# Kernel tuning notes

Hardware: AMD Instinct MI355X
Metric: run time of the kernel (lower is better)

## Reference

```python
import jax, jax.numpy as jnp
import numpy as np

D = 128; DFF = 256; NH = 4; HD = D // NH
B = 8; T = 1024
PAIRS = [(0, 1), (1, 2), (0, 2)]  # (ABSTRACT,DYNAMIC),(DYNAMIC,CONCRETE),(ABSTRACT,CONCRETE)
BW = 0.5 / 3.0   # bridge_weight / len(BRIDGE_PAIRS)
LB_W = 0.01


def _hex_np():
    # itertools.product([-1,1], repeat=6): index i = 6-bit binary of i, MSB first, 0->-1
    bits = (np.arange(64)[:, None] >> np.arange(5, -1, -1)) & 1
    return (bits * 2.0 - 1.0).astype(np.float32)


def _anchors_np():
    h = _hex_np()
    idx = {'GEO': 0, 'HYDRO': 18, 'PYRO': 45, 'AERO': 6, 'COSMO': 27, 'NOOS': 63}
    a = (h[idx['NOOS']] + h[idx['COSMO']]) / 2.0   # ABSTRACT
    d = (h[idx['AERO']] + h[idx['PYRO']]) / 2.0    # DYNAMIC
    c = (h[idx['GEO']] + h[idx['HYDRO']]) / 2.0    # CONCRETE
    return np.stack([a, d, c]).astype(np.float32)


def _ln(x, g, b, eps=1e-5):
    m = x.mean(-1, keepdims=True)
    v = ((x - m) ** 2).mean(-1, keepdims=True)
    return (x - m) * jax.lax.rsqrt(v + eps) * g + b


def _mha(q, kv, in_w, out_w):
    # torch nn.MultiheadAttention, bias=False, batch_first
    Bq, Tq, _ = q.shape
    wq, wk, wv = in_w[:D], in_w[D:2 * D], in_w[2 * D:]
    Q = (q @ wq.T).reshape(Bq, Tq, NH, HD)
    K = (kv @ wk.T).reshape(Bq, Tq, NH, HD)
    V = (kv @ wv.T).reshape(Bq, Tq, NH, HD)
    scores = jnp.einsum('bqhd,bkhd->bhqk', Q, K) / jnp.sqrt(jnp.float32(HD))
    attn = jax.nn.softmax(scores, axis=-1)
    o = jnp.einsum('bhqk,bkhd->bqhd', attn, V).reshape(Bq, Tq, D)
    return o @ out_w.T


def setup_inputs() -> dict:
    key = jax.random.key(0)
    ks = iter(jax.random.split(key, 40))
    r = lambda shape, s=0.02: jax.random.normal(next(ks), shape, dtype=jnp.float32) * s
    return {
        'x': jax.random.normal(next(ks), (B, T, D), dtype=jnp.float32),
        'gr_norm_g': jnp.ones((D,), jnp.float32), 'gr_norm_b': jnp.zeros((D,), jnp.float32),
        'q6_w': r((6, D), 0.1),
        'log_temp': jnp.log(jnp.float32(0.5)),
        'grp_norm_g': jnp.ones((3, D), jnp.float32), 'grp_norm_b': jnp.zeros((3, D), jnp.float32),
        'grp_proj_w': r((3, 2, D), 0.1), 'grp_proj_b': jnp.zeros((3, 2), jnp.float32),
        'me_norm_g': jnp.ones((6, D), jnp.float32), 'me_norm_b': jnp.zeros((6, D), jnp.float32),
        'me_gate_w': r((6, DFF, D)), 'me_val_w': r((6, DFF, D)), 'me_out_w': r((6, D, DFF)),
        'br_in_w': r((3, 3 * D, D)), 'br_out_w': r((3, D, D)),
        'br_nq_g': jnp.ones((3, D), jnp.float32), 'br_nq_b': jnp.zeros((3, D), jnp.float32),
        'br_nkv_g': jnp.ones((3, D), jnp.float32), 'br_nkv_b': jnp.zeros((3, D), jnp.float32),
        'br_nffn_g': jnp.ones((3, D), jnp.float32), 'br_nffn_b': jnp.zeros((3, D), jnp.float32),
        'br_gate_w': r((3, 2 * D, D)), 'br_val_w': r((3, 2 * D, D)), 'br_ffn_out_w': r((3, D, 2 * D)),
        'br_gate': jnp.full((3,), -2.0, dtype=jnp.float32),
        'out_norm_g': jnp.ones((D,), jnp.float32), 'out_norm_b': jnp.zeros((D,), jnp.float32),
        'out_w': r((D, D)),
    }


def reference(x, gr_norm_g, gr_norm_b, q6_w, log_temp, grp_norm_g, grp_norm_b,
              grp_proj_w, grp_proj_b, me_norm_g, me_norm_b, me_gate_w, me_val_w,
              me_out_w, br_in_w, br_out_w, br_nq_g, br_nq_b, br_nkv_g, br_nkv_b,
              br_nffn_g, br_nffn_b, br_gate_w, br_val_w, br_ffn_out_w, br_gate,
              out_norm_g, out_norm_b, out_w):
    hexg = jnp.asarray(_hex_np())        # (64, 6)
    anchors = jnp.asarray(_anchors_np())  # (3, 6)

    # ---- GlobalRouter ----
    h = _ln(x, gr_norm_g, gr_norm_b)
    soft_bits = jnp.tanh(h @ q6_w.T)                       # (B,T,6)
    sim = soft_bits @ hexg.T                               # (B,T,64)
    temp = jnp.clip(jnp.exp(log_temp), 0.1, 5.0)
    hex_w = jax.nn.softmax(sim / temp, axis=-1)
    soft_hex = hex_w @ hexg                                # (B,T,6)
    group_weights = jax.nn.softmax(soft_hex @ anchors.T, axis=-1)  # (B,T,3)
    mw = group_weights.mean(axis=(0, 1))
    lb_total = -(mw * jnp.log(mw + 1e-8)).sum()

    # ---- all 6 micro experts (per-expert LayerNorm shares x's stats) ----
    m = x.mean(-1, keepdims=True)
    v = ((x - m) ** 2).mean(-1, keepdims=True)
    xn = (x - m) * jax.lax.rsqrt(v + 1e-5)                 # (B,T,D)
    hme = xn[None] * me_norm_g[:, None, None, :] + me_norm_b[:, None, None, :]  # (6,B,T,D)
    gate = jax.nn.silu(jnp.einsum('ebtd,efd->ebtf', hme, me_gate_w))
    val = jnp.einsum('ebtd,efd->ebtf', hme, me_val_w)
    eo = jnp.einsum('ebtf,edf->ebtd', gate * val, me_out_w)  # (6,B,T,D)

    # ---- per-group routing (2 experts each, top_k=2) ----
    group_outs = []
    for g in range(3):  # groups ordered [ABSTRACT, DYNAMIC, CONCRETE]; experts [2g, 2g+1]
        hg = xn * grp_norm_g[g] + grp_norm_b[g]
        logits = hg @ grp_proj_w[g].T + grp_proj_b[g]      # (B,T,2)
        w = jax.nn.softmax(logits, axis=-1)
        vals, idx = jax.lax.top_k(w, 2)                    # k = min(top_k=2, n=2)
        sparse = (jax.nn.one_hot(idx, 2, dtype=w.dtype) * vals[..., None]).sum(-2)
        sparse = sparse / (sparse.sum(-1, keepdims=True) + 1e-8)
        mwg = w.mean(axis=(0, 1))
        lb_total = lb_total - (mwg * jnp.log(mwg + 1e-8)).sum()
        go = sparse[..., 0:1] * eo[2 * g] + sparse[..., 1:2] * eo[2 * g + 1]
        group_outs.append(group_weights[..., g:g + 1] * go)

    # ---- bridge experts ----
    bridge_sum = jnp.zeros_like(x)
    for i, (a, b) in enumerate(PAIRS):
        xq, xk = group_outs[a], group_outs[b]
        qn = _ln(xq, br_nq_g[i], br_nq_b[i])
        kvn = _ln(xk, br_nkv_g[i], br_nkv_b[i])
        xb = xq + _mha(qn, kvn, br_in_w[i], br_out_w[i])
        hb = _ln(xb, br_nffn_g[i], br_nffn_b[i])
        ff = (jax.nn.silu(hb @ br_gate_w[i].T) * (hb @ br_val_w[i].T)) @ br_ffn_out_w[i].T
        xb = (xb + ff) * jax.nn.sigmoid(br_gate[i])
        bridge_sum = bridge_sum + BW * xb

    combined = group_outs[0] + group_outs[1] + group_outs[2] + bridge_sum
    out = _ln(combined, out_norm_g, out_norm_b) @ out_w.T
    return out, lb_total * LB_W
```

## Files before the change

kernel.cpp:

```cpp
#include <hip/hip_runtime.h>
#include <math.h>

#define DD    128
#define DFF   256
#define NHH   4
#define HDD   32
#define BB    8
#define TT    1024
#define NTOK  (BB*TT)
#define LDK   72
#define QKVN  384

#define WB_MEGATE 0
#define WB_MEVAL  196608
#define WB_MEOUT  393216
#define WB_BRIN   589824
#define WB_BROUT  737280
#define WB_BRG    786432
#define WB_BRV    884736
#define WB_BRF    983040
#define WB_OUTW   1081344
#define WB_TOT    1097728

typedef __bf16 bf16x8 __attribute__((ext_vector_type(8)));
typedef float  f32x4  __attribute__((ext_vector_type(4)));

__device__ __forceinline__ float wsum(float v){
#pragma unroll
  for(int o=32;o>0;o>>=1) v += __shfl_xor(v,o,64);
  return v;
}
__device__ __forceinline__ float wmaxr(float v){
#pragma unroll
  for(int o=32;o>0;o>>=1) v = fmaxf(v,__shfl_xor(v,o,64));
  return v;
}
__device__ __forceinline__ unsigned short f2bf(float x){
  __bf16 h = (__bf16)x;
  unsigned short u;
  __builtin_memcpy(&u, &h, 2);
  return u;
}

__device__ __forceinline__ void stage16(const float* __restrict__ gp,
                                        unsigned short* __restrict__ dst){
  float4 f0 = *reinterpret_cast<const float4*>(gp);
  float4 f1 = *reinterpret_cast<const float4*>(gp+4);
  float4 f2 = *reinterpret_cast<const float4*>(gp+8);
  float4 f3 = *reinterpret_cast<const float4*>(gp+12);
  float f[16] = {f0.x,f0.y,f0.z,f0.w, f1.x,f1.y,f1.z,f1.w,
                 f2.x,f2.y,f2.z,f2.w, f3.x,f3.y,f3.z,f3.w};
  unsigned short h[16];
#pragma unroll
  for(int j=0;j<16;j++) h[j] = f2bf(f[j]);
  *reinterpret_cast<uint4*>(dst)   = *reinterpret_cast<const uint4*>(h);
  *reinterpret_cast<uint4*>(dst+8) = *reinterpret_cast<const uint4*>(h+8);
}

__device__ __forceinline__ void stage16bf(const unsigned short* __restrict__ gp,
                                          unsigned short* __restrict__ dst){
  const uint4* s = reinterpret_cast<const uint4*>(gp);
  *reinterpret_cast<uint4*>(dst)   = s[0];
  *reinterpret_cast<uint4*>(dst+8) = s[1];
}

__device__ __forceinline__ void stageLN(const float* __restrict__ fr,
                                        float mean, float rstd,
                                        const float* __restrict__ g,
                                        const float* __restrict__ b,
                                        unsigned short* __restrict__ dst){
  unsigned short h[16];
#pragma unroll
  for(int j=0;j<16;j++){
    float y = (fr[j]-mean)*rstd*g[j] + b[j];
    h[j] = f2bf(y);
  }
  *reinterpret_cast<uint4*>(dst)   = *reinterpret_cast<const uint4*>(h);
  *reinterpret_cast<uint4*>(dst+8) = *reinterpret_cast<const uint4*>(h+8);
}

__global__ __launch_bounds__(256) void wconv(
    const float* __restrict__ a0, const float* __restrict__ a1, const float* __restrict__ a2,
    const float* __restrict__ a3, const float* __restrict__ a4, const float* __restrict__ a5,
    const float* __restrict__ a6, const float* __restrict__ a7, const float* __restrict__ a8,
    unsigned short* __restrict__ dst, float qsc){
  size_t i = ((size_t)blockIdx.x*256 + threadIdx.x)*4;
  if(i >= WB_TOT) return;
  const float* s; size_t off = i; float sc = 1.0f;
  if(i < WB_MEVAL){ s=a0; }
  else if(i < WB_MEOUT){ s=a1; off = i-WB_MEVAL; }
  else if(i < WB_BRIN ){ s=a2; off = i-WB_MEOUT; }
  else if(i < WB_BROUT){ s=a3; off = i-WB_BRIN;
    int row = (int)(off>>7); if((row % 384) < 128) sc = qsc; }
  else if(i < WB_BRG ){ s=a4; off = i-WB_BROUT; }
  else if(i < WB_BRV ){ s=a5; off = i-WB_BRG; }
  else if(i < WB_BRF ){ s=a6; off = i-WB_BRV; }
  else if(i < WB_OUTW){ s=a7; off = i-WB_BRF; }
  else { s=a8; off = i-WB_OUTW; }
  float4 v = *reinterpret_cast<const float4*>(s + off);
  unsigned short h4[4] = {f2bf(v.x*sc), f2bf(v.y*sc), f2bf(v.z*sc), f2bf(v.w*sc)};
  *reinterpret_cast<uint2*>(dst + i) = *reinterpret_cast<const uint2*>(h4);
}

__global__ __launch_bounds__(256) void routing_kernel(
    const float* __restrict__ x,
    const float* __restrict__ gr_g, const float* __restrict__ gr_b,
    const float* __restrict__ q6,   const float* __restrict__ logtemp,
    const float* __restrict__ grp_g,const float* __restrict__ grp_b,
    const float* __restrict__ gpw,  const float* __restrict__ gpb,
    float* __restrict__ gw_out, float* __restrict__ coef, float* __restrict__ part){
  __shared__ float sp[4][9];
  int lane = threadIdx.x & 63;
  int wv   = threadIdx.x >> 6;
  int t    = (blockIdx.x<<2) + wv;
  const float* xr = x + (size_t)t*DD;
  float r0 = xr[lane], r1 = xr[lane+64];
  float mn = wsum(r0+r1) * (1.0f/DD);
  float d0 = r0-mn, d1 = r1-mn;
  float vv = wsum(d0*d0 + d1*d1) * (1.0f/DD);
  float rstd = rsqrtf(vv + 1e-5f);
  float x0 = d0*rstd, x1 = d1*rstd;
  float h0 = x0*gr_g[lane]+gr_b[lane];
  float h1 = x1*gr_g[lane+64]+gr_b[lane+64];
  float sb[6];
#pragma unroll
  for(int j=0;j<6;j++){
    float p = h0*q6[j*DD+lane] + h1*q6[j*DD+lane+64];
    sb[j] = tanhf(wsum(p));
  }
  float sim = 0.f;
#pragma unroll
  for(int j=0;j<6;j++) sim += ((lane>>(5-j))&1) ? sb[j] : -sb[j];
  float temp = expf(logtemp[0]); temp = fminf(fmaxf(temp,0.1f),5.0f);
  float mx = wmaxr(sim);
  float p  = expf((sim-mx)/temp);
  float w  = p / wsum(p);
  float sh[6];
#pragma unroll
  for(int j=0;j<6;j++) sh[j] = wsum(((lane>>(5-j))&1) ? w : -w);
  const float A0[6]={0,1,1,0,1,1}, A1[6]={0,-1,0,1,0,0}, A2[6]={-1,0,-1,-1,0,-1};
  float l0=0,l1=0,l2=0;
#pragma unroll
  for(int j=0;j<6;j++){ l0+=sh[j]*A0[j]; l1+=sh[j]*A1[j]; l2+=sh[j]*A2[j]; }
  float m3 = fmaxf(l0,fmaxf(l1,l2));
  float e0=expf(l0-m3), e1=expf(l1-m3), e2=expf(l2-m3);
  float inv3 = 1.0f/(e0+e1+e2);
  float g0=e0*inv3, g1=e1*inv3, g2=e2*inv3;
  if(lane==0){ gw_out[t*3]=g0; gw_out[t*3+1]=g1; gw_out[t*3+2]=g2; }
  float gwv[3]={g0,g1,g2};
  float pw[6];
#pragma unroll
  for(int g=0; g<3; g++){
    float hg0 = x0*grp_g[g*DD+lane]    + grp_b[g*DD+lane];
    float hg1 = x1*grp_g[g*DD+lane+64] + grp_b[g*DD+lane+64];
    float q0 = wsum(hg0*gpw[(g*2+0)*DD+lane] + hg1*gpw[(g*2+0)*DD+lane+64]) + gpb[g*2+0];
    float q1 = wsum(hg0*gpw[(g*2+1)*DD+lane] + hg1*gpw[(g*2+1)*DD+lane+64]) + gpb[g*2+1];
    float mm = fmaxf(q0,q1);
    float a0 = expf(q0-mm), a1 = expf(q1-mm);
    float inv = 1.0f/(a0+a1);
    float w0 = a0*inv, w1 = a1*inv;
    pw[g*2]=w0; pw[g*2+1]=w1;
    float invs = 1.0f/(w0+w1+1e-8f);
    if(lane==0){
      coef[(size_t)(2*g  )*NTOK + t] = gwv[g]*w0*invs;
      coef[(size_t)(2*g+1)*NTOK + t] = gwv[g]*w1*invs;
    }
  }
  if(lane==0){
    sp[wv][0]=g0; sp[wv][1]=g1; sp[wv][2]=g2;
#pragma unroll
    for(int k=0;k<6;k++) sp[wv][3+k]=pw[k];
  }
  __syncthreads();
  if(threadIdx.x<9){
    part[blockIdx.x*9+threadIdx.x] =
      sp[0][threadIdx.x]+sp[1][threadIdx.x]+sp[2][threadIdx.x]+sp[3][threadIdx.x];
  }
}

__global__ __launch_bounds__(256) void lb_kernel(const float* __restrict__ part, float* __restrict__ outlb){
  __shared__ float sm[4][9];
  float acc[9] = {};
  for(int i=threadIdx.x; i<2048; i+=256){
#pragma unroll
    for(int c=0;c<9;c++) acc[c] += part[i*9+c];
  }
#pragma unroll
  for(int c=0;c<9;c++) acc[c] = wsum(acc[c]);
  int wv = threadIdx.x>>6, lane = threadIdx.x&63;
  if(lane==0){
#pragma unroll
    for(int c=0;c<9;c++) sm[wv][c]=acc[c];
  }
  __syncthreads();
  if(threadIdx.x==0){
    const float invN = 1.0f/(float)NTOK;
    float lb=0;
#pragma unroll
    for(int c=0;c<9;c++){
      float s = sm[0][c]+sm[1][c]+sm[2][c]+sm[3][c];
      float mw = s*invN;
      lb -= mw*logf(mw+1e-8f);
    }
    outlb[0] = lb*0.01f;
  }
}

template<int MODE,int LN,int ABF,int OBF,int PSEL,int RSEL,int SUM,int QKV>
__global__ __launch_bounds__(256) void gemm_mfma(
    const void* __restrict__ Ap, const unsigned short* __restrict__ W, void* __restrict__ Cp,
    int M, int N, int K,
    const float* __restrict__ sv, const float* __restrict__ bv,
    const float* __restrict__ resid, const float* __restrict__ gptr,
    size_t az, size_t wz, size_t cz, size_t pz, size_t rz, size_t gz){
  __shared__ unsigned short As[64*LDK];
  __shared__ unsigned short Ws[64*LDK];
  const int z = blockIdx.z;
  const float* A = (const float*)Ap;
  const unsigned short* Ab = (const unsigned short*)Ap;
  if(QKV){
    bool isQ = (blockIdx.x < 2);
    int s = isQ ? ((z==1)?1:0) : ((z==0)?1:2);
    A += (size_t)s*NTOK*DD;
    if(!isQ){ sv = resid; bv = gptr; }
  } else if(PSEL==0){ A += z*az; Ab += z*az; }
  else if(PSEL==1){ int s = (z==1)?1:0; A += (size_t)s*NTOK*DD; Ab += (size_t)s*NTOK*DD; }
  else            { int s = (z==0)?1:2; A += (size_t)s*NTOK*DD; Ab += (size_t)s*NTOK*DD; }
  W += z*wz;
  float* C = (float*)Cp + z*cz;
  unsigned short* Cb = (unsigned short*)Cp + z*cz;
  const float* rs = resid;
  if(RSEL==0) rs += z*rz;
  else { int s = (z==1)?1:0; rs += (size_t)s*NTOK*DD; }
  sv += z*pz; bv += z*pz;
  const float* gp2 = gptr + z*gz;
  int tid  = threadIdx.x;
  int m0   = blockIdx.y*64, n0 = blockIdx.x*64;
  int w    = tid>>6, lane = tid&63;
  int wr   = (w>>1)*32, wc = (w&1)*32;
  int r    = tid>>2, seg = (tid&3)*16;
  f32x4 acc[2][2] = {};
  auto step = [&](){
#pragma unroll
    for(int kk=0;kk<64;kk+=32){
      int ko = kk + (lane>>4)*8;
      bf16x8 a0 = *reinterpret_cast<const bf16x8*>(&As[(wr    + (lane&15))*LDK + ko]);
      bf16x8 a1 = *reinterpret_cast<const bf16x8*>(&As[(wr+16 + (lane&15))*LDK + ko]);
      bf16x8 b0 = *reinterpret_cast<const bf16x8*>(&Ws[(wc    + (lane&15))*LDK + ko]);
      bf16x8 b1 = *reinterpret_cast<const bf16x8*>(&Ws[(wc+16 + (lane&15))*LDK + ko]);
      acc[0][0] = __builtin_amdgcn_mfma_f32_16x16x32_bf16(a0,b0,acc[0][0],0,0,0);
      acc[0][1] = __builtin_amdgcn_mfma_f32_16x16x32_bf16(a0,b1,acc[0][1],0,0,0);
      acc[1][0] = __builtin_amdgcn_mfma_f32_16x16x32_bf16(a1,b0,acc[1][0],0,0,0);
      acc[1][1] = __builtin_amdgcn_mfma_f32_16x16x32_bf16(a1,b1,acc[1][1],0,0,0);
    }
  };
  if(LN){
    float fr[32]; float mean, rstd;
    if(SUM){
#pragma unroll
      for(int j=0;j<32;j++) fr[j]=0.f;
#pragma unroll
      for(int s=0;s<3;s++){
        const float* r1 = A     + (size_t)s*NTOK*DD + (size_t)(m0+r)*K + seg;
        const float* r2 = resid + (size_t)s*NTOK*DD + (size_t)(m0+r)*K + seg;
#pragma unroll
        for(int j=0;j<4;j++){
          float4 v1 = *reinterpret_cast<const float4*>(r1 + j*4);
          float4 v2 = *reinterpret_cast<const float4*>(r2 + j*4);
          fr[j*4]+=v1.x+v2.x; fr[j*4+1]+=v1.y+v2.y; fr[j*4+2]+=v1.z+v2.z; fr[j*4+3]+=v1.w+v2.w;
          float4 w1 = *reinterpret_cast<const float4*>(r1 + 64 + j*4);
          float4 w2 = *reinterpret_cast<const float4*>(r2 + 64 + j*4);
          fr[16+j*4]+=w1.x+w2.x; fr[16+j*4+1]+=w1.y+w2.y; fr[16+j*4+2]+=w1.z+w2.z; fr[16+j*4+3]+=w1.w+w2.w;
        }
      }
    } else {
      const float* arow = A + (size_t)(m0+r)*K + seg;
#pragma unroll
      for(int j=0;j<4;j++) *reinterpret_cast<float4*>(&fr[j*4])    = *reinterpret_cast<const float4*>(arow + j*4);
#pragma unroll
      for(int j=0;j<4;j++) *reinterpret_cast<float4*>(&fr[16+j*4]) = *reinterpret_cast<const float4*>(arow + 64 + j*4);
    }
    float s1=0.f, s2=0.f;
#pragma unroll
    for(int j=0;j<32;j++){ s1 += fr[j]; s2 += fr[j]*fr[j]; }
    s1 += __shfl_xor(s1,1,64); s1 += __shfl_xor(s1,2,64);
    s2 += __shfl_xor(s2,1,64); s2 += __shfl_xor(s2,2,64);
    mean = s1*(1.0f/DD);
    float var = s2*(1.0f/DD) - mean*mean;
    rstd = rsqrtf(var + 1e-5f);
#pragma unroll
    for(int kh=0; kh<2; ++kh){
      __syncthreads();
      stageLN(fr + kh*16, mean, rstd, sv + kh*64 + seg, bv + kh*64 + seg, &As[r*LDK + seg]);
      stage16bf(W + (size_t)(n0+r)*K + kh*64 + seg, &Ws[r*LDK + seg]);
      __syncthreads();
      step();
    }
  } else {
    for(int k0=0;k0<K;k0+=64){
      __syncthreads();
      if(ABF) stage16bf(Ab + (size_t)(m0+r)*K + k0 + seg, &As[r*LDK + seg]);
      else    stage16(A  + (size_t)(m0+r)*K + k0 + seg, &As[r*LDK + seg]);
      stage16bf(W + (size_t)(n0+r)*K + k0 + seg, &Ws[r*LDK + seg]);
      __syncthreads();
      step();
    }
  }
#pragma unroll
  for(int i=0;i<2;i++){
#pragma unroll
    for(int j=0;j<2;j++){
      int mb = m0 + wr + i*16 + (lane>>4)*4;
      int n  = n0 + wc + j*16 + (lane&15);
#pragma unroll
      for(int rg=0;rg<4;rg++){
        int m = mb + rg;
        float v = acc[i][j][rg];
        size_t o = (size_t)m*N + n;
        if(MODE==0){ if(OBF) Cb[o] = f2bf(v); else C[o] = v; }
        else if(MODE==3){ C[o] = rs[o] + v; }
        else if(MODE==5){
          float gs = (0.5f/3.0f)/(1.0f+expf(-gp2[0]));
          C[o] = gs*(rs[o]+v);
        }
      }
    }
  }
}

__global__ __launch_bounds__(256) void gemm_dual(
    const float* __restrict__ A, const unsigned short* __restrict__ G,
    const unsigned short* __restrict__ V,
    unsigned short* __restrict__ C, int M, int N, int K,
    const float* __restrict__ sv, const float* __restrict__ bv,
    size_t az, size_t wz, size_t cz, size_t pz){
  __shared__ unsigned short As[64*LDK];
  __shared__ unsigned short Gs[64*LDK];
  __shared__ unsigned short Vs[64*LDK];
  const int z = blockIdx.z;
  A += z*az; G += z*wz; V += z*wz; C += z*cz; sv += z*pz; bv += z*pz;
  int tid  = threadIdx.x;
  int m0   = blockIdx.y*64, n0 = blockIdx.x*64;
  int w    = tid>>6, lane = tid&63;
  int wr   = (w>>1)*32, wc = (w&1)*32;
  int r    = tid>>2, seg = (tid&3)*16;
  f32x4 accg[2][2] = {};
  f32x4 accv[2][2] = {};
  float fr[32]; float mean, rstd;
  {
    const float* arow = A + (size_t)(m0+r)*K + seg;
#pragma unroll
    for(int j=0;j<4;j++) *reinterpret_cast<float4*>(&fr[j*4])    = *reinterpret_cast<const float4*>(arow + j*4);
#pragma unroll
    for(int j=0;j<4;j++) *reinterpret_cast<float4*>(&fr[16+j*4]) = *reinterpret_cast<const float4*>(arow + 64 + j*4);
    float s1=0.f, s2=0.f;
#pragma unroll
    for(int j=0;j<32;j++){ s1 += fr[j]; s2 += fr[j]*fr[j]; }
    s1 += __shfl_xor(s1,1,64); s1 += __shfl_xor(s1,2,64);
    s2 += __shfl_xor(s2,1,64); s2 += __shfl_xor(s2,2,64);
    mean = s1*(1.0f/DD);
    float var = s2*(1.0f/DD) - mean*mean;
    rstd = rsqrtf(var + 1e-5f);
  }
#pragma unroll
  for(int kh=0; kh<2; ++kh){
    int k0 = kh*64;
    __syncthreads();
    stageLN(fr + kh*16, mean, rstd, sv + k0 + seg, bv + k0 + seg, &As[r*LDK + seg]);
    stage16bf(G + (size_t)(n0+r)*K + k0 + seg, &Gs[r*LDK + seg]);
    stage16bf(V + (size_t)(n0+r)*K + k0 + seg, &Vs[r*LDK + seg]);
    __syncthreads();
#pragma unroll
    for(int kk=0;kk<64;kk+=32){
      int ko = kk + (lane>>4)*8;
      bf16x8 a0 = *reinterpret_cast<const bf16x8*>(&As[(wr    + (lane&15))*LDK + ko]);
      bf16x8 a1 = *reinterpret_cast<const bf16x8*>(&As[(wr+16 + (lane&15))*LDK + ko]);
      bf16x8 g0 = *reinterpret_cast<const bf16x8*>(&Gs[(wc    + (lane&15))*LDK + ko]);
      bf16x8 g1 = *reinterpret_cast<const bf16x8*>(&Gs[(wc+16 + (lane&15))*LDK + ko]);
      bf16x8 v0 = *reinterpret_cast<const bf16x8*>(&Vs[(wc    + (lane&15))*LDK + ko]);
      bf16x8 v1 = *reinterpret_cast<const bf16x8*>(&Vs[(wc+16 + (lane&15))*LDK + ko]);
      accg[0][0] = __builtin_amdgcn_mfma_f32_16x16x32_bf16(a0,g0,accg[0][0],0,0,0);
      accg[0][1] = __builtin_amdgcn_mfma_f32_16x16x32_bf16(a0,g1,accg[0][1],0,0,0);
      accg[1][0] = __builtin_amdgcn_mfma_f32_16x16x32_bf16(a1,g0,accg[1][0],0,0,0);
      accg[1][1] = __builtin_amdgcn_mfma_f32_16x16x32_bf16(a1,g1,accg[1][1],0,0,0);
      accv[0][0] = __builtin_amdgcn_mfma_f32_16x16x32_bf16(a0,v0,accv[0][0],0,0,0);
      accv[0][1] = __builtin_amdgcn_mfma_f32_16x16x32_bf16(a0,v1,accv[0][1],0,0,0);
      accv[1][0] = __builtin_amdgcn_mfma_f32_16x16x32_bf16(a1,v0,accv[1][0],0,0,0);
      accv[1][1] = __builtin_amdgcn_mfma_f32_16x16x32_bf16(a1,v1,accv[1][1],0,0,0);
    }
  }
#pragma unroll
  for(int i=0;i<2;i++){
#pragma unroll
    for(int j=0;j<2;j++){
      int mb = m0 + wr + i*16 + (lane>>4)*4;
      int n  = n0 + wc + j*16 + (lane&15);
#pragma unroll
      for(int rg=0;rg<4;rg++){
        float gg = accg[i][j][rg];
        float vv = accv[i][j][rg];
        float sg = gg/(1.0f+expf(-gg));
        C[(size_t)(mb+rg)*N + n] = f2bf(sg*vv);
      }
    }
  }
}

__global__ __launch_bounds__(256) void gemm_moe2(
    const unsigned short* __restrict__ Ab, const unsigned short* __restrict__ Wb,
    float* __restrict__ Cb, const float* __restrict__ coef){
  __shared__ unsigned short As0[64*LDK];
  __shared__ unsigned short As1[64*LDK];
  __shared__ unsigned short Ws0[64*LDK];
  __shared__ unsigned short Ws1[64*LDK];
  const int g = blockIdx.z;
  const unsigned short* A0 = Ab + (size_t)(2*g)*NTOK*DFF;
  const unsigned short* A1 = A0 + (size_t)NTOK*DFF;
  const unsigned short* W0 = Wb + (size_t)(2*g)*DD*DFF;
  const unsigned short* W1 = W0 + (size_t)DD*DFF;
  float* C = Cb + (size_t)g*NTOK*DD;
  const float* c0 = coef + (size_t)(2*g)*NTOK;
  const float* c1 = c0 + NTOK;
  int tid  = threadIdx.x;
  int m0   = blockIdx.y*64, n0 = blockIdx.x*64;
  int w    = tid>>6, lane = tid&63;
  int wr   = (w>>1)*32, wc = (w&1)*32;
  int r    = tid>>2, seg = (tid&3)*16;
  f32x4 a0acc[2][2] = {};
  f32x4 a1acc[2][2] = {};
  for(int k0=0;k0<DFF;k0+=64){
    __syncthreads();
    stage16bf(A0 + (size_t)(m0+r)*DFF + k0 + seg, &As0[r*LDK + seg]);
    stage16bf(A1 + (size_t)(m0+r)*DFF + k0 + seg, &As1[r*LDK + seg]);
    stage16bf(W0 + (size_t)(n0+r)*DFF + k0 + seg, &Ws0[r*LDK + seg]);
    stage16bf(W1 + (size_t)(n0+r)*DFF + k0 + seg, &Ws1[r*LDK + seg]);
    __syncthreads();
#pragma unroll
    for(int kk=0;kk<64;kk+=32){
      int ko = kk + (lane>>4)*8;
      bf16x8 x00 = *reinterpret_cast<const bf16x8*>(&As0[(wr    + (lane&15))*LDK + ko]);
      bf16x8 x01 = *reinterpret_cast<const bf16x8*>(&As0[(wr+16 + (lane&15))*LDK + ko]);
      bf16x8 x10 = *reinterpret_cast<const bf16x8*>(&As1[(wr    + (lane&15))*LDK + ko]);
      bf16x8 x11 = *reinterpret_cast<const bf16x8*>(&As1[(wr+16 + (lane&15))*LDK + ko]);
      bf16x8 w00 = *reinterpret_cast<const bf16x8*>(&Ws0[(wc    + (lane&15))*LDK + ko]);
      bf16x8 w01 = *reinterpret_cast<const bf16x8*>(&Ws0[(wc+16 + (lane&15))*LDK + ko]);
      bf16x8 w10 = *reinterpret_cast<const bf16x8*>(&Ws1[(wc    + (lane&15))*LDK + ko]);
      bf16x8 w11 = *reinterpret_cast<const bf16x8*>(&Ws1[(wc+16 + (lane&15))*LDK + ko]);
      a0acc[0][0] = __builtin_amdgcn_mfma_f32_16x16x32_bf16(x00,w00,a0acc[0][0],0,0,0);
      a0acc[0][1] = __builtin_amdgcn_mfma_f32_16x16x32_bf16(x00,w01,a0acc[0][1],0,0,0);
      a0acc[1][0] = __builtin_amdgcn_mfma_f32_16x16x32_bf16(x01,w00,a0acc[1][0],0,0,0);
      a0acc[1][1] = __builtin_amdgcn_mfma_f32_16x16x32_bf16(x01,w01,a0acc[1][1],0,0,0);
      a1acc[0][0] = __builtin_amdgcn_mfma_f32_16x16x32_bf16(x10,w10,a1acc[0][0],0,0,0);
      a1acc[0][1] = __builtin_amdgcn_mfma_f32_16x16x32_bf16(x10,w11,a1acc[0][1],0,0,0);
      a1acc[1][0] = __builtin_amdgcn_mfma_f32_16x16x32_bf16(x11,w10,a1acc[1][0],0,0,0);
      a1acc[1][1] = __builtin_amdgcn_mfma_f32_16x16x32_bf16(x11,w11,a1acc[1][1],0,0,0);
    }
  }
#pragma unroll
  for(int i=0;i<2;i++){
#pragma unroll
    for(int j=0;j<2;j++){
      int mb = m0 + wr + i*16 + (lane>>4)*4;
      int n  = n0 + wc + j*16 + (lane&15);
#pragma unroll
      for(int rg=0;rg<4;rg++){
        int m = mb + rg;
        C[(size_t)m*DD + n] = c0[m]*a0acc[i][j][rg] + c1[m]*a1acc[i][j][rg];
      }
    }
  }
}

#define PSW(row) (((row)&8)<<1)
#define VSW(row) ((((row)>>3)&3)<<3)
__global__ __launch_bounds__(256) void attn_fused(
    const unsigned short* __restrict__ qkv,
    unsigned short* __restrict__ obuf){
  __shared__ __align__(16) unsigned short Ks[64*40];
  __shared__ __align__(16) unsigned short Vt[48*72];
  __shared__ __align__(16) unsigned short Ps[4][16*72];
  const int tid = threadIdx.x;
  const int w = tid>>6, lane = tid&63;
  const int lr = lane&15, lg = lane>>4;
  const int n_  = blockIdx.x;
  const int kx  = n_ & 7, jx = n_ >> 3;
  const int grp = kx*12 + (jx>>4);
  const int bx  = jx & 15;
  const int h   = grp & 3;
  const int b   = (grp>>2) & 7;
  const int br  = grp >> 5;
  const int qtok0 = b*TT + bx*64 + w*16;
  for(int idx=tid; idx<16*72; idx+=256)
    Vt[32*72 + idx] = (idx < 64) ? (unsigned short)0x3F80 : (unsigned short)0;
  const unsigned short* qp = qkv + (size_t)br*NTOK*QKVN + (size_t)(qtok0 + lr)*QKVN + h*HDD + lg*8;
  bf16x8 qa = *reinterpret_cast<const bf16x8*>(qp);
  f32x4 o0 = {}, o1 = {}, o2 = {};
  float m[4] = {-1e30f,-1e30f,-1e30f,-1e30f};
  const unsigned short* KVbase = qkv + (size_t)br*NTOK*QKVN + (size_t)(b*TT)*QKVN + DD + h*HDD;

  for(int t0=0; t0<TT; t0+=64){
    __syncthreads();
#pragma unroll
    for(int s2=0;s2<2;s2++){
      int i   = tid + s2*256;
      int key = i>>3, seg = (i&7)*4;
      const unsigned short* src = KVbase + (size_t)(t0+key)*QKVN + seg;
      *reinterpret_cast<uint2*>(&Ks[key*40+seg]) = *reinterpret_cast<const uint2*>(src);
      unsigned short vs[4];
      *reinterpret_cast<uint2*>(vs) = *reinterpret_cast<const uint2*>(src + DD);
      const int kc = key ^ VSW(seg);
      Vt[(seg  )*72+kc] = vs[0];
      Vt[(seg+1)*72+kc] = vs[1];
      Vt[(seg+2)*72+kc] = vs[2];
      Vt[(seg+3)*72+kc] = vs[3];
    }
    __syncthreads();
    f32x4 s[4];
#pragma unroll
    for(int f=0;f<4;f++){
      bf16x8 kb = *reinterpret_cast<const bf16x8*>(&Ks[(f*16+lr)*40 + lg*8]);
      f32x4 z = {};
      s[f] = __builtin_amdgcn_mfma_f32_16x16x32_bf16(qa,kb,z,0,0,0);
    }
    float tmax[4]; bool need=false;
#pragma unroll
    for(int r=0;r<4;r++){
      tmax[r] = fmaxf(fmaxf(s[0][r],s[1][r]),fmaxf(s[2][r],s[3][r]));
      need = need || (tmax[r] > m[r] + 8.0f);
    }
    if(__any(need)){
#pragma unroll
      for(int r=0;r<4;r++){
        float t = tmax[r];
#pragma unroll
        for(int off=1;off<16;off<<=1) t = fmaxf(t,__shfl_xor(t,off,64));
        float nm = fmaxf(m[r],t);
        float sc = __builtin_amdgcn_exp2f(m[r]-nm);
        m[r] = nm; o0[r] *= sc; o1[r] *= sc; o2[r] *= sc;
      }
    }
#pragma unroll
    for(int r=0;r<4;r++){
      const int q = lg*4+r;
      const int cw = PSW(q);
#pragma unroll
      for(int f=0;f<4;f++){
        float p = __builtin_amdgcn_exp2f(s[f][r]-m[r]);
        Ps[w][q*72 + ((f*16+lr)^cw)] = f2bf(p);
      }
    }
    const int pw_ = PSW(lr);
    bf16x8 pa0 = *reinterpret_cast<const bf16x8*>(&Ps[w][lr*72 + ((lg*8   )^pw_)]);
    bf16x8 pa1 = *reinterpret_cast<const bf16x8*>(&Ps[w][lr*72 + ((lg*8+32)^pw_)]);
    {
      const int r_ = lr, vw = VSW(r_);
      bf16x8 vb0 = *reinterpret_cast<const bf16x8*>(&Vt[r_*72 + ((lg*8   )^vw)]);
      bf16x8 vb1 = *reinterpret_cast<const bf16x8*>(&Vt[r_*72 + ((lg*8+32)^vw)]);
      o0 = __builtin_amdgcn_mfma_f32_16x16x32_bf16(pa0,vb0,o0,0,0,0);
      o0 = __builtin_amdgcn_mfma_f32_16x16x32_bf16(pa1,vb1,o0,0,0,0);
    }
    {
      const int r_ = 16+lr, vw = VSW(r_);
      bf16x8 vb0 = *reinterpret_cast<const bf16x8*>(&Vt[r_*72 + ((lg*8   )^vw)]);
      bf16x8 vb1 = *reinterpret_cast<const bf16x8*>(&Vt[r_*72 + ((lg*8+32)^vw)]);
      o1 = __builtin_amdgcn_mfma_f32_16x16x32_bf16(pa0,vb0,o1,0,0,0);
      o1 = __builtin_amdgcn_mfma_f32_16x16x32_bf16(pa1,vb1,o1,0,0,0);
    }
    {
      const int r_ = 32+lr, vw = VSW(r_);
      bf16x8 vb0 = *reinterpret_cast<const bf16x8*>(&Vt[r_*72 + ((lg*8   )^vw)]);
      bf16x8 vb1 = *reinterpret_cast<const bf16x8*>(&Vt[r_*72 + ((lg*8+32)^vw)]);
      o2 = __builtin_amdgcn_mfma_f32_16x16x32_bf16(pa0,vb0,o2,0,0,0);
      o2 = __builtin_amdgcn_mfma_f32_16x16x32_bf16(pa1,vb1,o2,0,0,0);
    }
  }
#pragma unroll
  for(int r=0;r<4;r++){
    float lsr = __shfl(o2[r], lane & 48, 64);
    float inv = 1.0f/lsr;
    int row = qtok0 + lg*4 + r;
    unsigned short* orow = obuf + (size_t)br*NTOK*DD + (size_t)row*DD + h*HDD;
    orow[lr]    = f2bf(o0[r]*inv);
    orow[16+lr] = f2bf(o1[r]*inv);
  }
}

extern "C" void kernel_launch(void* const* d_in, const int* in_sizes, int n_in,
                              void* d_out, int out_size, void* d_ws, size_t ws_size,
                              hipStream_t stream){
  (void)in_sizes; (void)n_in; (void)out_size; (void)ws_size;
  const float* x       = (const float*)d_in[0];
  const float* gr_g    = (const float*)d_in[1];
  const float* gr_b    = (const float*)d_in[2];
  const float* q6_w    = (const float*)d_in[3];
  const float* logtemp = (const float*)d_in[4];
  const float* grp_g   = (const float*)d_in[5];
  const float* grp_b   = (const float*)d_in[6];
  const float* gpw     = (const float*)d_in[7];
  const float* gpb     = (const float*)d_in[8];
  const float* me_g    = (const float*)d_in[9];
  const float* me_b    = (const float*)d_in[10];
  const float* me_gate = (const float*)d_in[11];
  const float* me_val  = (const float*)d_in[12];
  const float* me_out  = (const float*)d_in[13];
  const float* br_in   = (const float*)d_in[14];
  const float* br_outw = (const float*)d_in[15];
  const float* nq_g    = (const float*)d_in[16];
  const float* nq_b    = (const float*)d_in[17];
  const float* nkv_g   = (const float*)d_in[18];
  const float* nkv_b   = (const float*)d_in[19];
  const float* nff_g   = (const float*)d_in[20];
  const float* nff_b   = (const float*)d_in[21];
  const float* brg_w   = (const float*)d_in[22];
  const float* brv_w   = (const float*)d_in[23];
  const float* brf_w   = (const float*)d_in[24];
  const float* br_gate = (const float*)d_in[25];
  const float* on_g    = (const float*)d_in[26];
  const float* on_b    = (const float*)d_in[27];
  const float* out_w   = (const float*)d_in[28];
  float* out = (float*)d_out;
  float* ws  = (float*)d_ws;

  float* coef  = ws;
  float* part  = ws + 65536;
  unsigned short* gvb6 = (unsigned short*)(ws + 131072);
  float* go    = ws + 6731072;
  unsigned short* qkv  = (unsigned short*)(ws + 9900000);
  unsigned short* obuf = (unsigned short*)(ws + 14700000);
  unsigned short* wbf  = (unsigned short*)(ws + 21400000);
  float* xb    = ws + 23000000;
  unsigned short* gvb2 = (unsigned short*)(ws + 26200000);
  float* bsum  = ws + 29400000;
  float* gw    = ws + 32700000;

  const float qscale = 0.17677669529663687f * 1.4426950408889634f;

  wconv<<<1072,256,0,stream>>>(me_gate, me_val, me_out, br_in, br_outw,
                               brg_w, brv_w, brf_w, out_w, wbf, qscale);

  routing_kernel<<<2048,256,0,stream>>>(x, gr_g, gr_b, q6_w, logtemp,
                                        grp_g, grp_b, gpw, gpb, gw, coef, part);
  lb_kernel<<<1,256,0,stream>>>(part, out + 1048576);

  gemm_dual<<<dim3(4,128,6),256,0,stream>>>(x, wbf+WB_MEGATE, wbf+WB_MEVAL, gvb6,
      NTOK,DFF,DD, me_g, me_b, 0, (size_t)DFF*DD, (size_t)NTOK*DFF, DD);
  gemm_moe2<<<dim3(2,128,3),256,0,stream>>>(gvb6, wbf+WB_MEOUT, go, coef);

  gemm_mfma<0,1,0,1,0,0,0,1><<<dim3(6,128,3),256,0,stream>>>(go, wbf+WB_BRIN, qkv,
      NTOK,QKVN,DD, nq_g, nq_b, nkv_g, nkv_b,
      0, (size_t)QKVN*DD, (size_t)NTOK*QKVN, DD, 0, 0);
  attn_fused<<<1536,256,0,stream>>>(qkv, obuf);
  gemm_mfma<3,0,1,0,0,1,0,0><<<dim3(2,128,3),256,0,stream>>>(obuf, wbf+WB_BROUT, xb,
      NTOK,DD,DD, nullptr, nullptr, go, nullptr,
      (size_t)NTOK*DD, (size_t)DD*DD, (size_t)NTOK*DD, 0, 0, 0);
  gemm_dual<<<dim3(4,128,3),256,0,stream>>>(xb, wbf+WB_BRG, wbf+WB_BRV, gvb2,
      NTOK,2*DD,DD, nff_g, nff_b, (size_t)NTOK*DD, (size_t)2*DD*DD, (size_t)NTOK*2*DD, DD);
  gemm_mfma<5,0,1,0,0,0,0,0><<<dim3(2,128,3),256,0,stream>>>(gvb2, wbf+WB_BRF, bsum,
      NTOK,DD,2*DD, nullptr, nullptr, xb, br_gate,
      (size_t)NTOK*2*DD, (size_t)DD*2*DD, (size_t)NTOK*DD, 0, (size_t)NTOK*DD, 1);

  gemm_mfma<0,1,0,0,0,0,1,0><<<dim3(2,128,1),256,0,stream>>>(go, wbf+WB_OUTW, out,
      NTOK,DD,DD, on_g, on_b, bsum, nullptr,
      0, 0, 0, 0, 0, 0);
}
```

Baseline: 193.5 us.

## Double-buffer K/V tiles in attention kernel with register prefetch

The attention kernel now keeps two shared-memory buffers for K and transposed V. Each iteration issues the global loads for the next tile into registers, computes on the current buffer, then writes the prefetched tile into the other buffer. This cuts the per-tile sync pair down to one barrier and overlaps global load latency with MFMA and softmax work. The cost is more LDS and more live registers, which may reduce occupancy. The ones block used for the row-sum column moves into its own array.

```diff
diff --git a/kernel.cpp b/kernel.cpp
--- a/kernel.cpp
+++ b/kernel.cpp
@@ -476,8 +476,9 @@
 __global__ __launch_bounds__(256) void attn_fused(
     const unsigned short* __restrict__ qkv,
     unsigned short* __restrict__ obuf){
-  __shared__ __align__(16) unsigned short Ks[64*40];
-  __shared__ __align__(16) unsigned short Vt[48*72];
+  __shared__ __align__(16) unsigned short Ks[2][64*40];
+  __shared__ __align__(16) unsigned short Vt[2][32*72];
+  __shared__ __align__(16) unsigned short Vones[16*72];
   __shared__ __align__(16) unsigned short Ps[4][16*72];
   const int tid = threadIdx.x;
   const int w = tid>>6, lane = tid&63;
@@ -491,34 +492,51 @@
   const int br  = grp >> 5;
   const int qtok0 = b*TT + bx*64 + w*16;
   for(int idx=tid; idx<16*72; idx+=256)
-    Vt[32*72 + idx] = (idx < 64) ? (unsigned short)0x3F80 : (unsigned short)0;
+    Vones[idx] = (idx < 64) ? (unsigned short)0x3F80 : (unsigned short)0;
   const unsigned short* qp = qkv + (size_t)br*NTOK*QKVN + (size_t)(qtok0 + lr)*QKVN + h*HDD + lg*8;
   bf16x8 qa = *reinterpret_cast<const bf16x8*>(qp);
   f32x4 o0 = {}, o1 = {}, o2 = {};
   float m[4] = {-1e30f,-1e30f,-1e30f,-1e30f};
   const unsigned short* KVbase = qkv + (size_t)br*NTOK*QKVN + (size_t)(b*TT)*QKVN + DD + h*HDD;
-
-  for(int t0=0; t0<TT; t0+=64){
-    __syncthreads();
-#pragma unroll
-    for(int s2=0;s2<2;s2++){
-      int i   = tid + s2*256;
-      int key = i>>3, seg = (i&7)*4;
-      const unsigned short* src = KVbase + (size_t)(t0+key)*QKVN + seg;
-      *reinterpret_cast<uint2*>(&Ks[key*40+seg]) = *reinterpret_cast<const uint2*>(src);
-      unsigned short vs[4];
-      *reinterpret_cast<uint2*>(vs) = *reinterpret_cast<const uint2*>(src + DD);
-      const int kc = key ^ VSW(seg);
-      Vt[(seg  )*72+kc] = vs[0];
-      Vt[(seg+1)*72+kc] = vs[1];
-      Vt[(seg+2)*72+kc] = vs[2];
-      Vt[(seg+3)*72+kc] = vs[3];
-    }
-    __syncthreads();
+  const int skey0 = (tid    )>>3, sseg0 = ((tid    )&7)*4;
+  const int skey1 = (tid+256)>>3, sseg1 = ((tid+256)&7)*4;
+
+  {
+    const unsigned short* s0 = KVbase + (size_t)skey0*QKVN + sseg0;
+    const unsigned short* s1 = KVbase + (size_t)skey1*QKVN + sseg1;
+    uint2 k0v = *reinterpret_cast<const uint2*>(s0);
+    uint2 v0v = *reinterpret_cast<const uint2*>(s0 + DD);
+    uint2 k1v = *reinterpret_cast<const uint2*>(s1);
+    uint2 v1v = *reinterpret_cast<const uint2*>(s1 + DD);
+    *reinterpret_cast<uint2*>(&Ks[0][skey0*40+sseg0]) = k0v;
+    *reinterpret_cast<uint2*>(&Ks[0][skey1*40+sseg1]) = k1v;
+    unsigned short vs[4];
+    *reinterpret_cast<uint2*>(vs) = v0v;
+    { const int kc = skey0 ^ VSW(sseg0);
+      Vt[0][(sseg0  )*72+kc]=vs[0]; Vt[0][(sseg0+1)*72+kc]=vs[1];
+      Vt[0][(sseg0+2)*72+kc]=vs[2]; Vt[0][(sseg0+3)*72+kc]=vs[3]; }
+    *reinterpret_cast<uint2*>(vs) = v1v;
+    { const int kc = skey1 ^ VSW(sseg1);
+      Vt[0][(sseg1  )*72+kc]=vs[0]; Vt[0][(sseg1+1)*72+kc]=vs[1];
+      Vt[0][(sseg1+2)*72+kc]=vs[2]; Vt[0][(sseg1+3)*72+kc]=vs[3]; }
+  }
+  __syncthreads();
+
+  for(int t=0; t<16; t++){
+    const int cur = t & 1;
+    uint2 kn0, vn0, kn1, vn1;
+    if(t < 15){
+      const unsigned short* s0 = KVbase + (size_t)((t+1)*64 + skey0)*QKVN + sseg0;
+      const unsigned short* s1 = KVbase + (size_t)((t+1)*64 + skey1)*QKVN + sseg1;
+      kn0 = *reinterpret_cast<const uint2*>(s0);
+      vn0 = *reinterpret_cast<const uint2*>(s0 + DD);
+      kn1 = *reinterpret_cast<const uint2*>(s1);
+      vn1 = *reinterpret_cast<const uint2*>(s1 + DD);
+    }
     f32x4 s[4];
 #pragma unroll
     for(int f=0;f<4;f++){
-      bf16x8 kb = *reinterpret_cast<const bf16x8*>(&Ks[(f*16+lr)*40 + lg*8]);
+      bf16x8 kb = *reinterpret_cast<const bf16x8*>(&Ks[cur][(f*16+lr)*40 + lg*8]);
       f32x4 z = {};
       s[f] = __builtin_amdgcn_mfma_f32_16x16x32_bf16(qa,kb,z,0,0,0);
     }
@@ -531,10 +549,10 @@
     if(__any(need)){
 #pragma unroll
       for(int r=0;r<4;r++){
-        float t = tmax[r];
-#pragma unroll
-        for(int off=1;off<16;off<<=1) t = fmaxf(t,__shfl_xor(t,off,64));
-        float nm = fmaxf(m[r],t);
+        float t2 = tmax[r];
+#pragma unroll
+        for(int off=1;off<16;off<<=1) t2 = fmaxf(t2,__shfl_xor(t2,off,64));
+        float nm = fmaxf(m[r],t2);
         float sc = __builtin_amdgcn_exp2f(m[r]-nm);
         m[r] = nm; o0[r] *= sc; o1[r] *= sc; o2[r] *= sc;
       }
@@ -554,25 +572,40 @@
     bf16x8 pa1 = *reinterpret_cast<const bf16x8*>(&Ps[w][lr*72 + ((lg*8+32)^pw_)]);
     {
       const int r_ = lr, vw = VSW(r_);
-      bf16x8 vb0 = *reinterpret_cast<const bf16x8*>(&Vt[r_*72 + ((lg*8   )^vw)]);
-      bf16x8 vb1 = *reinterpret_cast<const bf16x8*>(&Vt[r_*72 + ((lg*8+32)^vw)]);
+      bf16x8 vb0 = *reinterpret_cast<const bf16x8*>(&Vt[cur][r_*72 + ((lg*8   )^vw)]);
+      bf16x8 vb1 = *reinterpret_cast<const bf16x8*>(&Vt[cur][r_*72 + ((lg*8+32)^vw)]);
       o0 = __builtin_amdgcn_mfma_f32_16x16x32_bf16(pa0,vb0,o0,0,0,0);
       o0 = __builtin_amdgcn_mfma_f32_16x16x32_bf16(pa1,vb1,o0,0,0,0);
     }
     {
       const int r_ = 16+lr, vw = VSW(r_);
-      bf16x8 vb0 = *reinterpret_cast<const bf16x8*>(&Vt[r_*72 + ((lg*8   )^vw)]);
-      bf16x8 vb1 = *reinterpret_cast<const bf16x8*>(&Vt[r_*72 + ((lg*8+32)^vw)]);
+      bf16x8 vb0 = *reinterpret_cast<const bf16x8*>(&Vt[cur][(r_-16)*72 + ((lg*8   )^vw)+16*72]);
+      bf16x8 vb1 = *reinterpret_cast<const bf16x8*>(&Vt[cur][(r_-16)*72 + ((lg*8+32)^vw)+16*72]);
       o1 = __builtin_amdgcn_mfma_f32_16x16x32_bf16(pa0,vb0,o1,0,0,0);
       o1 = __builtin_amdgcn_mfma_f32_16x16x32_bf16(pa1,vb1,o1,0,0,0);
     }
     {
       const int r_ = 32+lr, vw = VSW(r_);
-      bf16x8 vb0 = *reinterpret_cast<const bf16x8*>(&Vt[r_*72 + ((lg*8   )^vw)]);
-      bf16x8 vb1 = *reinterpret_cast<const bf16x8*>(&Vt[r_*72 + ((lg*8+32)^vw)]);
+      bf16x8 vb0 = *reinterpret_cast<const bf16x8*>(&Vones[lr*72 + ((lg*8   )^vw)]);
+      bf16x8 vb1 = *reinterpret_cast<const bf16x8*>(&Vones[lr*72 + ((lg*8+32)^vw)]);
       o2 = __builtin_amdgcn_mfma_f32_16x16x32_bf16(pa0,vb0,o2,0,0,0);
       o2 = __builtin_amdgcn_mfma_f32_16x16x32_bf16(pa1,vb1,o2,0,0,0);
     }
+    if(t < 15){
+      const int nb = cur ^ 1;
+      *reinterpret_cast<uint2*>(&Ks[nb][skey0*40+sseg0]) = kn0;
+      *reinterpret_cast<uint2*>(&Ks[nb][skey1*40+sseg1]) = kn1;
+      unsigned short vs[4];
+      *reinterpret_cast<uint2*>(vs) = vn0;
+      { const int kc = skey0 ^ VSW(sseg0);
+        Vt[nb][(sseg0  )*72+kc]=vs[0]; Vt[nb][(sseg0+1)*72+kc]=vs[1];
+        Vt[nb][(sseg0+2)*72+kc]=vs[2]; Vt[nb][(sseg0+3)*72+kc]=vs[3]; }
+      *reinterpret_cast<uint2*>(vs) = vn1;
+      { const int kc = skey1 ^ VSW(sseg1);
+        Vt[nb][(sseg1  )*72+kc]=vs[0]; Vt[nb][(sseg1+1)*72+kc]=vs[1];
+        Vt[nb][(sseg1+2)*72+kc]=vs[2]; Vt[nb][(sseg1+3)*72+kc]=vs[3]; }
+    }
+    __syncthreads();
   }
 #pragma unroll
   for(int r=0;r<4;r++){
```

Result: no change. 191.1 us (-1.3%).
